# Kernel optimization log

Measured on AMD Instinct MI355X. Metric: run time of the kernel, lower is better.

Reference implementation:

```python
import jax, jax.numpy as jnp
import numpy as np

BLOCK = 64


def setup_inputs() -> dict:
    key = jax.random.key(0)
    ks = jax.random.split(key, 8)
    B, S, H = 16, 2048, 768
    E, M, P = 32, 4, 128
    L = 97
    return {
        "task_features": jax.random.normal(ks[0], (B, S, H), dtype=jnp.float32),
        "entity_position_ids": jax.random.randint(ks[1], (B, E, M), 0, S),
        "head_tail_idxs": jax.random.randint(ks[2], (B, P, 2), 0, E),
        "Wh": jax.random.normal(ks[3], (H, H), dtype=jnp.float32) * 0.02,
        "bh": jnp.zeros((H,), dtype=jnp.float32),
        "Wt": jax.random.normal(ks[4], (H, H), dtype=jnp.float32) * 0.02,
        "bt": jnp.zeros((H,), dtype=jnp.float32),
        "Wc": jax.random.normal(ks[5], (H * BLOCK, L), dtype=jnp.float32) * 0.02,
        "bc": jnp.zeros((L,), dtype=jnp.float32),
    }


def reference(task_features, entity_position_ids, head_tail_idxs, Wh, bh, Wt, bt, Wc, bc):
    B, S, H = task_features.shape
    pos = entity_position_ids  # [B, E, M] mention start positions
    # One-hot semantics: indicator[start]=1, so duplicate mention positions within an
    # entity count once. Keep only first occurrence of each position per entity.
    eq = pos[..., :, None] == pos[..., None, :]          # [B, E, M, M]
    dup = jnp.any(jnp.tril(eq, -1), axis=-1)             # equal to an earlier mention
    w = (~dup).astype(task_features.dtype)               # [B, E, M]
    # Gather mention-start features and pool (sum) per entity: [B, E, H]
    feats = task_features[jnp.arange(B)[:, None, None], pos]  # [B, E, M, H]
    ent = jnp.einsum('bemh,bem->beh', feats, w)
    # Select subject/object entity representations per pair
    bi = jnp.arange(B)[:, None]
    subj = ent[bi, head_tail_idxs[..., 0]].reshape(-1, H)  # [B*P, H]
    obj = ent[bi, head_tail_idxs[..., 1]].reshape(-1, H)
    z_s = jnp.tanh(subj @ Wh + bh)
    z_o = jnp.tanh(obj @ Wt + bt)
    N = z_s.shape[0]
    b1 = z_s.reshape(N, H // BLOCK, BLOCK)
    b2 = z_o.reshape(N, H // BLOCK, BLOCK)
    # Block-bilinear: per-block outer product -> [N, H*BLOCK]
    bl = (b1[..., :, None] * b2[..., None, :]).reshape(N, H * BLOCK)
    logits = bl @ Wc + bc  # [N, 97]
    return logits
```

## Files before the change

kernel.cpp:

```cpp
#include <hip/hip_runtime.h>
#include <hip/hip_bf16.h>

typedef __bf16 bf16_t;
typedef bf16_t bf16x8 __attribute__((ext_vector_type(8)));
typedef float  f32x4  __attribute__((ext_vector_type(4)));

#define B_    16
#define S_    2048
#define H_    768
#define E_    32
#define M_    4
#define P_    128
#define L_    97
#define NPAIR 2048
#define RSPLIT 48

#define OFF_WHT  0u
#define OFF_WTT  (OFF_WHT + 768u*768u*2u)
#define OFF_WCG  (OFF_WTT + 768u*768u*2u)
#define OFF_ENT  (OFF_WCG + 768u*14336u)
#define OFF_ZS   (OFF_ENT + 512u*768u*2u)
#define OFF_ZO   (OFF_ZS  + 512u*768u*2u)
#define OFF_PART (OFF_ZO  + 512u*768u*2u)

typedef __attribute__((address_space(1))) const unsigned gu32;
typedef __attribute__((address_space(3))) unsigned lu32;

static __device__ __forceinline__ float bf_lo(unsigned u) { return __builtin_bit_cast(float, u << 16); }
static __device__ __forceinline__ float bf_hi(unsigned u) { return __builtin_bit_cast(float, u & 0xffff0000u); }
static __device__ __forceinline__ unsigned short bf_bits(float f) {
    return __builtin_bit_cast(unsigned short, (bf16_t)f);
}

__global__ __launch_bounds__(256) void k_prep(const float* __restrict__ Wh,
                                              const float* __restrict__ Wt,
                                              const float* __restrict__ Wc,
                                              const float* __restrict__ tf,
                                              const int* __restrict__ pos,
                                              bf16_t* __restrict__ whT,
                                              bf16_t* __restrict__ wtT,
                                              unsigned* __restrict__ wcg,
                                              bf16_t* __restrict__ ent) {
    int bid = blockIdx.x;
    if (bid < 1152) {
        __shared__ float tile[32][33];
        int z   = bid / 576;
        int rem = bid - z * 576;
        const float* W = z ? Wt : Wh;
        bf16_t* WT = z ? wtT : whT;
        int k0 = (rem % 24) * 32, c0 = (rem / 24) * 32;
        int tx = threadIdx.x & 31, ty = threadIdx.x >> 5;
        for (int r = 0; r < 4; r++) {
            int ky = ty + r * 8;
            tile[ky][tx] = W[(k0 + ky) * H_ + c0 + tx];
        }
        __syncthreads();
        for (int r = 0; r < 4; r++) {
            int cy = ty + r * 8;
            WT[(c0 + cy) * H_ + (k0 + tx)] = (bf16_t)tile[tx][cy];
        }
    } else if (bid < 1920) {
        int I = bid - 1152;
        unsigned base_dw = (unsigned)I * 3584u;
        for (int r = 0; r < 14; r++) {
            int d  = threadIdx.x + 256 * r;
            int l  = d >> 5;
            int gp = (d >> 2) & 7;
            int k  = d & 3;
            int gl = gp ^ (l & 7);
            int j  = (gl * 4 + k) * 2;
            int p  = I * 64 + j;
            float v0 = (l < L_) ? Wc[(size_t)p * L_ + l]       : 0.f;
            float v1 = (l < L_) ? Wc[(size_t)(p + 1) * L_ + l] : 0.f;
            unsigned pk = (unsigned)bf_bits(v0) | ((unsigned)bf_bits(v1) << 16);
            wcg[base_dw + d] = pk;
        }
    } else {
        int be = bid - 1920;
        int b  = be >> 5;
        int p0 = pos[be*4+0], p1 = pos[be*4+1], p2 = pos[be*4+2], p3 = pos[be*4+3];
        bool w1 = (p1 != p0);
        bool w2 = (p2 != p0) && (p2 != p1);
        bool w3 = (p3 != p0) && (p3 != p1) && (p3 != p2);
        const float* base = tf + (size_t)b * S_ * H_;
        for (int qq = 0; qq < 3; qq++) {
            int h = threadIdx.x + qq * 256;
            float s = base[(size_t)p0 * H_ + h];
            if (w1) s += base[(size_t)p1 * H_ + h];
            if (w2) s += base[(size_t)p2 * H_ + h];
            if (w3) s += base[(size_t)p3 * H_ + h];
            ent[(size_t)be * H_ + h] = (bf16_t)s;
        }
    }
}

__global__ __launch_bounds__(256) void k_gemm_z(const bf16_t* __restrict__ ent,
                                                const bf16_t* __restrict__ whT,
                                                const bf16_t* __restrict__ wtT,
                                                const float* __restrict__ bh,
                                                const float* __restrict__ bt,
                                                bf16_t* __restrict__ zs,
                                                bf16_t* __restrict__ zo) {
    const bf16_t* WT  = blockIdx.z ? wtT : whT;
    const float* bias = blockIdx.z ? bt  : bh;
    bf16_t* outp      = blockIdx.z ? zo  : zs;
    int w = threadIdx.x >> 6, lane = threadIdx.x & 63;
    int ml = lane & 15, q = lane >> 4;
    int m0 = blockIdx.x * 64 + w * 16;
    int c0 = blockIdx.y * 64;
    f32x4 zero4 = {0.f, 0.f, 0.f, 0.f};
    f32x4 acc[4] = {zero4, zero4, zero4, zero4};
    const bf16_t* aptr = ent + (size_t)(m0 + ml) * H_ + q * 8;
    for (int kk = 0; kk < 24; kk++) {
        bf16x8 a = *reinterpret_cast<const bf16x8*>(aptr + kk * 32);
        for (int lt = 0; lt < 4; lt++) {
            const bf16_t* bp = WT + (size_t)(c0 + lt * 16 + ml) * H_ + kk * 32 + q * 8;
            bf16x8 bfr = *reinterpret_cast<const bf16x8*>(bp);
            acc[lt] = __builtin_amdgcn_mfma_f32_16x16x32_bf16(a, bfr, acc[lt], 0, 0, 0);
        }
    }
    for (int lt = 0; lt < 4; lt++)
        for (int r = 0; r < 4; r++) {
            int row = q * 4 + r;
            int col = c0 + lt * 16 + ml;
            float v = tanhf(acc[lt][r] + bias[col]);
            outp[(size_t)(m0 + row) * H_ + col] = (bf16_t)v;
        }
}

__global__ __launch_bounds__(512, 3) void k_bilinear(const bf16_t* __restrict__ zs,
                                                     const bf16_t* __restrict__ zo,
                                                     const unsigned* __restrict__ wcg,
                                                     const int* __restrict__ ht,
                                                     float* __restrict__ pout) {
    __shared__ __align__(16) unsigned wc_lds[2][112 * 32];
    __shared__ unsigned short zs_lds[16 * 256];
    int nb = blockIdx.x;
    int c  = blockIdx.y;
    int I0 = c * 16;
    int kblk = I0 >> 6;
    int i0   = I0 & 63;
    int t = threadIdx.x;
    int w = t >> 6, lane = t & 63, ml = lane & 15, q = lane >> 4;
    int nbase = nb * 256;

    if (t < 256) {
        int n  = nbase + t;
        int es = (n >> 7) * E_ + ht[n * 2 + 0];
        const unsigned short* src =
            reinterpret_cast<const unsigned short*>(zs) + (size_t)es * H_ + kblk * 64 + i0;
        uint4 u0 = *reinterpret_cast<const uint4*>(src);
        uint4 u1 = *reinterpret_cast<const uint4*>(src + 8);
        unsigned vals[8] = {u0.x, u0.y, u0.z, u0.w, u1.x, u1.y, u1.z, u1.w};
        for (int d = 0; d < 8; d++) {
            zs_lds[(2 * d) * 256 + t]     = (unsigned short)(vals[d] & 0xffffu);
            zs_lds[(2 * d + 1) * 256 + t] = (unsigned short)(vals[d] >> 16);
        }
    }

    bf16x8 zoA[2][2];
    for (int nt = 0; nt < 2; nt++) {
        int n  = nbase + (w * 2 + nt) * 16 + ml;
        int eo = (n >> 7) * E_ + ht[n * 2 + 1];
        const bf16_t* src = zo + (size_t)eo * H_ + kblk * 64;
        zoA[nt][0] = *reinterpret_cast<const bf16x8*>(src + 0 * 32 + q * 8);
        zoA[nt][1] = *reinterpret_cast<const bf16x8*>(src + 1 * 32 + q * 8);
    }

    f32x4 zero4 = {0.f, 0.f, 0.f, 0.f};
    f32x4 acc[2][7];
    for (int nt = 0; nt < 2; nt++)
        for (int lt = 0; lt < 7; lt++) acc[nt][lt] = zero4;

    const unsigned* gsrc = wcg + (size_t)I0 * 3584u;

    for (int pp = w; pp < 14; pp += 8)
        __builtin_amdgcn_global_load_lds((gu32*)(gsrc + pp * 256 + lane * 4),
                                         (lu32*)&wc_lds[0][pp * 256], 16, 0, 0);
    __syncthreads();

    int sw = ml & 7;
    for (int ii = 0; ii < 16; ii++) {
        int pb = ii & 1;
        if (ii < 15) {
            const unsigned* g2 = gsrc + (size_t)(ii + 1) * 3584u;
            for (int pp = w; pp < 14; pp += 8)
                __builtin_amdgcn_global_load_lds((gu32*)(g2 + pp * 256 + lane * 4),
                                                 (lu32*)&wc_lds[1 - pb][pp * 256], 16, 0, 0);
        }

        float zsv[2][4];
        for (int nt = 0; nt < 2; nt++) {
            const unsigned* zp = reinterpret_cast<const unsigned*>(
                &zs_lds[ii * 256 + (w * 2 + nt) * 16 + q * 4]);
            unsigned z0 = zp[0], z1 = zp[1];
            zsv[nt][0] = bf_lo(z0); zsv[nt][1] = bf_hi(z0);
            zsv[nt][2] = bf_lo(z1); zsv[nt][3] = bf_hi(z1);
        }

        const unsigned short* wch = reinterpret_cast<const unsigned short*>(wc_lds[pb]);
        for (int lt = 0; lt < 7; lt++) {
            int l = lt * 16 + ml;
            bf16x8 b0 = *reinterpret_cast<const bf16x8*>(wch + l * 64 + ((q ^ sw) * 8));
            bf16x8 b1 = *reinterpret_cast<const bf16x8*>(wch + l * 64 + (((4 + q) ^ sw) * 8));
            for (int nt = 0; nt < 2; nt++) {
                f32x4 dres = __builtin_amdgcn_mfma_f32_16x16x32_bf16(zoA[nt][0], b0, zero4, 0, 0, 0);
                dres = __builtin_amdgcn_mfma_f32_16x16x32_bf16(zoA[nt][1], b1, dres, 0, 0, 0);
                for (int r = 0; r < 4; r++) acc[nt][lt][r] += zsv[nt][r] * dres[r];
            }
        }
        __syncthreads();
    }

    float* po = pout + ((size_t)c * NPAIR + nbase) * 112;
    for (int nt = 0; nt < 2; nt++)
        for (int lt = 0; lt < 7; lt++)
            for (int r = 0; r < 4; r++) {
                int nl = (w * 2 + nt) * 16 + q * 4 + r;
                po[(size_t)nl * 112 + lt * 16 + ml] = acc[nt][lt][r];
            }
}

__global__ __launch_bounds__(256) void k_reduce(const float* __restrict__ part,
                                                const float* __restrict__ bc,
                                                float* __restrict__ out) {
    int t = blockIdx.x * 256 + threadIdx.x;
    if (t >= NPAIR * 28) return;
    int n  = t / 28;
    int l4 = (t - n * 28) * 4;
    const float* p = part + (size_t)n * 112 + l4;
    f32x4 s = {0.f, 0.f, 0.f, 0.f};
    #pragma unroll
    for (int cc = 0; cc < RSPLIT; cc++) {
        f32x4 v = *reinterpret_cast<const f32x4*>(p + (size_t)cc * NPAIR * 112);
        s += v;
    }
    #pragma unroll
    for (int e = 0; e < 4; e++) {
        int l = l4 + e;
        if (l < L_) out[(size_t)n * L_ + l] = s[e] + bc[l];
    }
}

extern "C" void kernel_launch(void* const* d_in, const int* in_sizes, int n_in,
                              void* d_out, int out_size, void* d_ws, size_t ws_size,
                              hipStream_t stream) {
    (void)in_sizes; (void)n_in; (void)out_size; (void)ws_size;
    const float* tf  = (const float*)d_in[0];
    const int*   pos = (const int*)d_in[1];
    const int*   ht  = (const int*)d_in[2];
    const float* Wh  = (const float*)d_in[3];
    const float* bh  = (const float*)d_in[4];
    const float* Wt  = (const float*)d_in[5];
    const float* bt  = (const float*)d_in[6];
    const float* Wc  = (const float*)d_in[7];
    const float* bc  = (const float*)d_in[8];
    float* out = (float*)d_out;
    char*  ws  = (char*)d_ws;

    bf16_t*   whT  = (bf16_t*)(ws + OFF_WHT);
    bf16_t*   wtT  = (bf16_t*)(ws + OFF_WTT);
    unsigned* wcg  = (unsigned*)(ws + OFF_WCG);
    bf16_t*   ent  = (bf16_t*)(ws + OFF_ENT);
    bf16_t*   zsp  = (bf16_t*)(ws + OFF_ZS);
    bf16_t*   zop  = (bf16_t*)(ws + OFF_ZO);
    float*    part = (float*)(ws + OFF_PART);

    k_prep    <<<dim3(2432), 256, 0, stream>>>(Wh, Wt, Wc, tf, pos, whT, wtT, wcg, ent);
    k_gemm_z  <<<dim3(8, 12, 2), 256, 0, stream>>>(ent, whT, wtT, bh, bt, zsp, zop);
    k_bilinear<<<dim3(8, RSPLIT), 512, 0, stream>>>(zsp, zop, wcg, ht, part);
    k_reduce  <<<dim3((NPAIR * 28 + 255) / 256), 256, 0, stream>>>(part, bc, out);
}
```

Before: 230.5 us.

## Halve bilinear block width, store partials as bf16 in label-major layout

The bilinear kernel moves from 512 to 256 threads per block, so each wave handles four pair tiles instead of two, doubling the register accumulators and the reuse of each Wc fragment loaded from LDS. Partial sums are packed to bf16 and written in a [split][label][pair] layout, and the reduce kernel is rewritten to read that layout and accumulate in fp32. This halves partial-buffer traffic for both the writer and the reducer. In exchange it loses precision in the 48-way partial sums, and the larger register footprint may lower occupancy.

```diff
diff --git a/kernel.cpp b/kernel.cpp
--- a/kernel.cpp
+++ b/kernel.cpp
@@ -128,11 +128,11 @@
         }
 }
 
-__global__ __launch_bounds__(512, 3) void k_bilinear(const bf16_t* __restrict__ zs,
+__global__ __launch_bounds__(256, 2) void k_bilinear(const bf16_t* __restrict__ zs,
                                                      const bf16_t* __restrict__ zo,
                                                      const unsigned* __restrict__ wcg,
                                                      const int* __restrict__ ht,
-                                                     float* __restrict__ pout) {
+                                                     unsigned* __restrict__ pout) {
     __shared__ __align__(16) unsigned wc_lds[2][112 * 32];
     __shared__ unsigned short zs_lds[16 * 256];
     int nb = blockIdx.x;
@@ -144,7 +144,7 @@
     int w = t >> 6, lane = t & 63, ml = lane & 15, q = lane >> 4;
     int nbase = nb * 256;
 
-    if (t < 256) {
+    {
         int n  = nbase + t;
         int es = (n >> 7) * E_ + ht[n * 2 + 0];
         const unsigned short* src =
@@ -158,9 +158,9 @@
         }
     }
 
-    bf16x8 zoA[2][2];
-    for (int nt = 0; nt < 2; nt++) {
-        int n  = nbase + (w * 2 + nt) * 16 + ml;
+    bf16x8 zoA[4][2];
+    for (int nt = 0; nt < 4; nt++) {
+        int n  = nbase + (w * 4 + nt) * 16 + ml;
         int eo = (n >> 7) * E_ + ht[n * 2 + 1];
         const bf16_t* src = zo + (size_t)eo * H_ + kblk * 64;
         zoA[nt][0] = *reinterpret_cast<const bf16x8*>(src + 0 * 32 + q * 8);
@@ -168,13 +168,13 @@
     }
 
     f32x4 zero4 = {0.f, 0.f, 0.f, 0.f};
-    f32x4 acc[2][7];
-    for (int nt = 0; nt < 2; nt++)
+    f32x4 acc[4][7];
+    for (int nt = 0; nt < 4; nt++)
         for (int lt = 0; lt < 7; lt++) acc[nt][lt] = zero4;
 
     const unsigned* gsrc = wcg + (size_t)I0 * 3584u;
 
-    for (int pp = w; pp < 14; pp += 8)
+    for (int pp = w; pp < 14; pp += 4)
         __builtin_amdgcn_global_load_lds((gu32*)(gsrc + pp * 256 + lane * 4),
                                          (lu32*)&wc_lds[0][pp * 256], 16, 0, 0);
     __syncthreads();
@@ -184,15 +184,15 @@
         int pb = ii & 1;
         if (ii < 15) {
             const unsigned* g2 = gsrc + (size_t)(ii + 1) * 3584u;
-            for (int pp = w; pp < 14; pp += 8)
+            for (int pp = w; pp < 14; pp += 4)
                 __builtin_amdgcn_global_load_lds((gu32*)(g2 + pp * 256 + lane * 4),
                                                  (lu32*)&wc_lds[1 - pb][pp * 256], 16, 0, 0);
         }
 
-        float zsv[2][4];
-        for (int nt = 0; nt < 2; nt++) {
+        float zsv[4][4];
+        for (int nt = 0; nt < 4; nt++) {
             const unsigned* zp = reinterpret_cast<const unsigned*>(
-                &zs_lds[ii * 256 + (w * 2 + nt) * 16 + q * 4]);
+                &zs_lds[ii * 256 + (w * 4 + nt) * 16 + q * 4]);
             unsigned z0 = zp[0], z1 = zp[1];
             zsv[nt][0] = bf_lo(z0); zsv[nt][1] = bf_hi(z0);
             zsv[nt][2] = bf_lo(z1); zsv[nt][3] = bf_hi(z1);
@@ -203,7 +203,7 @@
             int l = lt * 16 + ml;
             bf16x8 b0 = *reinterpret_cast<const bf16x8*>(wch + l * 64 + ((q ^ sw) * 8));
             bf16x8 b1 = *reinterpret_cast<const bf16x8*>(wch + l * 64 + (((4 + q) ^ sw) * 8));
-            for (int nt = 0; nt < 2; nt++) {
+            for (int nt = 0; nt < 4; nt++) {
                 f32x4 dres = __builtin_amdgcn_mfma_f32_16x16x32_bf16(zoA[nt][0], b0, zero4, 0, 0, 0);
                 dres = __builtin_amdgcn_mfma_f32_16x16x32_bf16(zoA[nt][1], b1, dres, 0, 0, 0);
                 for (int r = 0; r < 4; r++) acc[nt][lt][r] += zsv[nt][r] * dres[r];
@@ -212,34 +212,37 @@
         __syncthreads();
     }
 
-    float* po = pout + ((size_t)c * NPAIR + nbase) * 112;
-    for (int nt = 0; nt < 2; nt++)
-        for (int lt = 0; lt < 7; lt++)
-            for (int r = 0; r < 4; r++) {
-                int nl = (w * 2 + nt) * 16 + q * 4 + r;
-                po[(size_t)nl * 112 + lt * 16 + ml] = acc[nt][lt][r];
-            }
-}
-
-__global__ __launch_bounds__(256) void k_reduce(const float* __restrict__ part,
+    for (int nt = 0; nt < 4; nt++) {
+        int n0 = nbase + (w * 4 + nt) * 16 + q * 4;
+        for (int lt = 0; lt < 7; lt++) {
+            int l = lt * 16 + ml;
+            unsigned d0 = (unsigned)bf_bits(acc[nt][lt][0]) | ((unsigned)bf_bits(acc[nt][lt][1]) << 16);
+            unsigned d1 = (unsigned)bf_bits(acc[nt][lt][2]) | ((unsigned)bf_bits(acc[nt][lt][3]) << 16);
+            uint2 pk = {d0, d1};
+            *reinterpret_cast<uint2*>(pout + (((size_t)c * 112 + l) * NPAIR + n0) / 2) = pk;
+        }
+    }
+}
+
+__global__ __launch_bounds__(256) void k_reduce(const unsigned* __restrict__ part,
                                                 const float* __restrict__ bc,
                                                 float* __restrict__ out) {
     int t = blockIdx.x * 256 + threadIdx.x;
-    if (t >= NPAIR * 28) return;
-    int n  = t / 28;
-    int l4 = (t - n * 28) * 4;
-    const float* p = part + (size_t)n * 112 + l4;
+    if (t >= L_ * (NPAIR / 4)) return;
+    int n4 = t & 511;
+    int l  = t >> 9;
+    const unsigned* p = part + (size_t)l * (NPAIR / 2) + n4 * 2;
     f32x4 s = {0.f, 0.f, 0.f, 0.f};
     #pragma unroll
     for (int cc = 0; cc < RSPLIT; cc++) {
-        f32x4 v = *reinterpret_cast<const f32x4*>(p + (size_t)cc * NPAIR * 112);
-        s += v;
-    }
+        uint2 v = *reinterpret_cast<const uint2*>(p + (size_t)cc * 112 * (NPAIR / 2));
+        s[0] += bf_lo(v.x); s[1] += bf_hi(v.x);
+        s[2] += bf_lo(v.y); s[3] += bf_hi(v.y);
+    }
+    float b = bc[l];
     #pragma unroll
-    for (int e = 0; e < 4; e++) {
-        int l = l4 + e;
-        if (l < L_) out[(size_t)n * L_ + l] = s[e] + bc[l];
-    }
+    for (int e = 0; e < 4; e++)
+        out[(size_t)(n4 * 4 + e) * L_ + l] = s[e] + b;
 }
 
 extern "C" void kernel_launch(void* const* d_in, const int* in_sizes, int n_in,
@@ -264,10 +267,10 @@
     bf16_t*   ent  = (bf16_t*)(ws + OFF_ENT);
     bf16_t*   zsp  = (bf16_t*)(ws + OFF_ZS);
     bf16_t*   zop  = (bf16_t*)(ws + OFF_ZO);
-    float*    part = (float*)(ws + OFF_PART);
+    unsigned* part = (unsigned*)(ws + OFF_PART);
 
     k_prep    <<<dim3(2432), 256, 0, stream>>>(Wh, Wt, Wc, tf, pos, whT, wtT, wcg, ent);
     k_gemm_z  <<<dim3(8, 12, 2), 256, 0, stream>>>(ent, whT, wtT, bh, bt, zsp, zop);
-    k_bilinear<<<dim3(8, RSPLIT), 512, 0, stream>>>(zsp, zop, wcg, ht, part);
-    k_reduce  <<<dim3((NPAIR * 28 + 255) / 256), 256, 0, stream>>>(part, bc, out);
-}
+    k_bilinear<<<dim3(8, RSPLIT), 256, 0, stream>>>(zsp, zop, wcg, ht, part);
+    k_reduce  <<<dim3((L_ * (NPAIR / 4) + 255) / 256), 256, 0, stream>>>(part, bc, out);
+}
```

After: 222.9 us (median of 2 runs). -3.3%, faster.
